# Optimization experiments

Measured on AMD Instinct MI355X. Metric: run time of the kernel, lower is better.

The kernel has to match this reference:

```python
import jax, jax.numpy as jnp
import numpy as np

N_HEAD = 16

def _rope_cos_sin(T, head_dim, dtype):
    # inv_freq over even indices, freqs [T, head_dim//2]
    inv_freq = 1.0 / (10000.0 ** (jnp.arange(0, head_dim, 2, dtype=jnp.float32) / head_dim))
    t = jnp.arange(T, dtype=jnp.float32)
    freqs = t[:, None] * inv_freq[None, :]
    cos = jnp.cos(freqs).astype(dtype)[None, :, None, :]  # [1,T,1,hd/2]
    sin = jnp.sin(freqs).astype(dtype)[None, :, None, :]
    return cos, sin

def _apply_rope(x, cos, sin):
    # x: [B,T,H,hd]; interleaved halves as in the torch module
    x1, x2 = x[..., ::2], x[..., 1::2]
    return jnp.concatenate([x1 * cos - x2 * sin, x1 * sin + x2 * cos], axis=-1)

def setup_inputs() -> dict:
    key = jax.random.key(0)
    k1, k2, k3 = jax.random.split(key, 3)
    B, T, C = 2, 2048, 1024
    x = jax.random.normal(k1, (B, T, C), dtype=jnp.float32)
    # causal mask (mask==0 positions get -inf), broadcast over B and heads
    attn_mask = jnp.tril(jnp.ones((T, T), dtype=bool))[None, None, :, :]
    w_qkv = jax.random.normal(k2, (C, 3 * C), dtype=jnp.float32) * (1.0 / np.sqrt(C))
    w_out = jax.random.normal(k3, (C, C), dtype=jnp.float32) * (1.0 / np.sqrt(C))
    return {"x": x, "attn_mask": attn_mask, "w_qkv": w_qkv, "w_out": w_out}

def reference(x, attn_mask, w_qkv, w_out):
    B, T, C = x.shape
    H = N_HEAD
    hd = C // H
    qkv = x @ w_qkv  # [B,T,3C]
    q, k, v = jnp.split(qkv, 3, axis=2)
    q = q.reshape(B, T, H, hd)
    k = k.reshape(B, T, H, hd)
    v = v.reshape(B, T, H, hd)
    cos, sin = _rope_cos_sin(T, hd, x.dtype)
    q = _apply_rope(q, cos, sin)
    k = _apply_rope(k, cos, sin)
    scale = 1.0 / np.sqrt(hd).astype(np.float32)
    att = jnp.einsum('bthd,bshd->bhts', q, k) * scale  # [B,H,T,T]
    att = jnp.where(attn_mask, att, -jnp.inf)
    att = jax.nn.softmax(att, axis=-1)
    out = jnp.einsum('bhts,bshd->bthd', att, v).reshape(B, T, C)
    out = out @ w_out
    k_t = jnp.transpose(k, (0, 2, 1, 3))  # [B,H,T,hd]
    v_t = jnp.transpose(v, (0, 2, 1, 3))
    return out, k_t, v_t
```

## Files before the change

kernel.cpp:

```cpp
#include <hip/hip_runtime.h>

#define T_SEQ 2048
#define NH    16
#define HD    64
#define CDIM  1024
#define BDIM  2

using floatx4 = __attribute__((ext_vector_type(4))) float;
using bf16x8  = __attribute__((ext_vector_type(8))) __bf16;
using half4   = __attribute__((ext_vector_type(4))) _Float16;
using half8   = __attribute__((ext_vector_type(8))) _Float16;
typedef unsigned short u16;

__device__ __forceinline__ u16 f2bf(float f) {
  unsigned int u = __float_as_uint(f);
  u += 0x7fffu + ((u >> 16) & 1u);
  return (u16)(u >> 16);
}
__device__ __forceinline__ float bf2f(u16 h) {
  return __uint_as_float(((unsigned int)h) << 16);
}
__device__ __forceinline__ u16 f2h(float f) {
  union { _Float16 h; u16 u; } c; c.h = (_Float16)f; return c.u;
}
__device__ __forceinline__ unsigned pk2h(float a, float b) {
  return __builtin_bit_cast(unsigned, __builtin_amdgcn_cvt_pkrtz(a, b));
}
__device__ __forceinline__ void gld16(const void* g, const void* l) {
  __builtin_amdgcn_global_load_lds(
      (const __attribute__((address_space(1))) unsigned int*)(unsigned long long)g,
      (__attribute__((address_space(3))) unsigned int*)(unsigned int)(unsigned long long)l,
      16, 0, 0);
}

__global__ __launch_bounds__(256) void preproc(const float* __restrict__ x,
                                               const float* __restrict__ w_qkv,
                                               const float* __restrict__ w_out,
                                               u16* __restrict__ xb,
                                               u16* __restrict__ wqT,
                                               u16* __restrict__ woT) {
  __shared__ float tile[32][33];
  int blk = blockIdx.x, tid = threadIdx.x;
  if (blk < 4096) {
    int i = blk * 256 + tid;
    float4 v = ((const float4*)x)[i];
    ushort4 o;
    o.x = f2bf(v.x); o.y = f2bf(v.y); o.z = f2bf(v.z); o.w = f2bf(v.w);
    ((ushort4*)xb)[i] = o;
    return;
  }
  const float* W; u16* WT; int K, N, bx, by;
  if (blk < 4096 + 3072) {
    int idx = blk - 4096; W = w_qkv; WT = wqT; K = 1024; N = 3072;
    bx = idx % 96; by = idx / 96;
  } else {
    int idx = blk - 7168; W = w_out; WT = woT; K = 1024; N = 1024;
    bx = idx & 31; by = idx >> 5;
  }
  int n0 = bx * 32, k0 = by * 32;
  int tx = tid & 31, ty = tid >> 5;
#pragma unroll
  for (int i = 0; i < 32; i += 8)
    tile[ty + i][tx] = W[(size_t)(k0 + ty + i) * N + n0 + tx];
  __syncthreads();
#pragma unroll
  for (int i = 0; i < 32; i += 8)
    WT[(size_t)(n0 + ty + i) * K + k0 + tx] = f2bf(tile[tx][ty + i]);
}

template <bool OUT_F32>
__global__ __launch_bounds__(256) void gemm_bt(const u16* __restrict__ A,
                                               const u16* __restrict__ BT,
                                               float* __restrict__ Cf,
                                               u16* __restrict__ Cb,
                                               int M, int N, int K) {
  __shared__ u16 As[2][128 * 32];
  __shared__ u16 Bs[2][128 * 32];
  const int tid  = threadIdx.x;
  const int lane = tid & 63, wave = tid >> 6;
  const int quad = lane >> 4, l16 = lane & 15;
  const int wm = (wave & 1) * 64, wn = (wave >> 1) * 64;
  const int row0 = blockIdx.x * 128, col0 = blockIdx.y * 128;
  const int srow = tid >> 2;
  const int sc   = tid & 3;
  const int sgc  = (sc ^ ((srow >> 1) & 3)) * 8;
  floatx4 acc[4][4] = {};

  auto stage = [&](int buf, int k0) {
    gld16(A  + (size_t)(row0 + srow     ) * K + k0 + sgc, &As[buf][srow * 32 + sc * 8]);
    gld16(A  + (size_t)(row0 + srow + 64) * K + k0 + sgc, &As[buf][(srow + 64) * 32 + sc * 8]);
    gld16(BT + (size_t)(col0 + srow     ) * K + k0 + sgc, &Bs[buf][srow * 32 + sc * 8]);
    gld16(BT + (size_t)(col0 + srow + 64) * K + k0 + sgc, &Bs[buf][(srow + 64) * 32 + sc * 8]);
  };

  const int nk = K >> 5;
  stage(0, 0);
  for (int ki = 0; ki < nk; ki++) {
    const int cur = ki & 1;
    __builtin_amdgcn_s_barrier();
    int kn = ki + 1 < nk ? ki + 1 : nk - 1;
    stage(cur ^ 1, kn << 5);
    asm volatile("s_waitcnt vmcnt(4)" ::: "memory");
    __builtin_amdgcn_s_barrier();
    bf16x8 af[4], bfv[4];
#pragma unroll
    for (int mt = 0; mt < 4; mt++) {
      int r = wm + mt * 16 + l16;
      af[mt] = *(const bf16x8*)&As[cur][r * 32 + (quad ^ ((r >> 1) & 3)) * 8];
    }
#pragma unroll
    for (int nt = 0; nt < 4; nt++) {
      int r = wn + nt * 16 + l16;
      bfv[nt] = *(const bf16x8*)&Bs[cur][r * 32 + (quad ^ ((r >> 1) & 3)) * 8];
    }
#pragma unroll
    for (int mt = 0; mt < 4; mt++)
#pragma unroll
      for (int nt = 0; nt < 4; nt++)
        acc[mt][nt] = __builtin_amdgcn_mfma_f32_16x16x32_bf16(af[mt], bfv[nt], acc[mt][nt], 0, 0, 0);
  }
  asm volatile("s_waitcnt vmcnt(0)" ::: "memory");
#pragma unroll
  for (int mt = 0; mt < 4; mt++)
#pragma unroll
    for (int nt = 0; nt < 4; nt++)
#pragma unroll
      for (int r = 0; r < 4; r++) {
        int row = row0 + wm + mt * 16 + quad * 4 + r;
        int col = col0 + wn + nt * 16 + l16;
        float v = acc[mt][nt][r];
        if (OUT_F32) Cf[(size_t)row * N + col] = v;
        else         Cb[(size_t)row * N + col] = f2bf(v);
      }
}

__global__ __launch_bounds__(256) void rope_vpack(const u16* __restrict__ qkv,
                                                  u16* __restrict__ qf16,
                                                  u16* __restrict__ kf16,
                                                  float* __restrict__ kt_out,
                                                  float* __restrict__ vt_out,
                                                  u16* __restrict__ vtf) {
  int blk = blockIdx.x;
  if (blk < 16384) {
    int gid = blk * 4 + (threadIdx.x >> 6);
    int d   = threadIdx.x & 63;
    int t   = gid & (T_SEQ - 1);
    int h   = (gid >> 11) & 15;
    int b   = gid >> 15;
    const u16* qrow = qkv + ((size_t)(b * T_SEQ + t)) * 3072 + h * 64;
    int i = d & 31;
    unsigned int qp = *(const unsigned int*)(qrow + 2 * i);
    unsigned int kp = *(const unsigned int*)(qrow + 1024 + 2 * i);
    float q1 = bf2f((u16)qp), q2 = bf2f((u16)(qp >> 16));
    float k1 = bf2f((u16)kp), k2 = bf2f((u16)(kp >> 16));
    float inv = expf((float)i * -0.28782313662425572f);
    float ang = (float)t * inv;
    float sn = sinf(ang), cs = cosf(ang);
    float qv = (d < 32) ? (q1 * cs - q2 * sn) : (q1 * sn + q2 * cs);
    float kv = (d < 32) ? (k1 * cs - k2 * sn) : (k1 * sn + k2 * cs);
    size_t o = (size_t)gid * 64 + d;
    qf16[o] = f2h(qv * 0.18033688011112042f);
    kf16[o] = f2h(kv);
    kt_out[o] = kv;
    return;
  }
  __shared__ float tile[64][65];
  int b2 = blk - 16384;
  int t0 = (b2 & 31) * 64;
  int bh = b2 >> 5;
  int b = bh >> 4, h = bh & 15;
  int tx = threadIdx.x & 63, ty = threadIdx.x >> 6;
#pragma unroll
  for (int i = ty; i < 64; i += 4) {
    float v = bf2f(qkv[((size_t)(b * T_SEQ + t0 + i)) * 3072 + 2048 + h * 64 + tx]);
    tile[i][tx] = v;
    vt_out[((size_t)bh * T_SEQ + t0 + i) * 64 + tx] = v;
  }
  __syncthreads();
#pragma unroll
  for (int i = ty; i < 64; i += 4)
    vtf[((size_t)bh * 64 + i) * T_SEQ + t0 + tx] = f2h(tile[tx][i]);
}

__device__ __forceinline__ void qk_dual(const u16* Ks, const half8* qfA, const half8* qfB,
                                        floatx4 (&sA)[8], floatx4 (&sB)[8],
                                        int quad, int l16) {
#pragma unroll
  for (int kc = 0; kc < 2; kc++)
#pragma unroll
    for (int st = 0; st < 8; st++) {
      int srow = st * 16 + l16;
      half8 ak = *(const half8*)&Ks[srow * 64 + (((kc * 4 + quad) ^ (srow & 7)) * 8)];
      sA[st] = __builtin_amdgcn_mfma_f32_16x16x32_f16(ak, qfA[kc], sA[st], 0, 0, 0);
      sB[st] = __builtin_amdgcn_mfma_f32_16x16x32_f16(ak, qfB[kc], sB[st], 0, 0, 0);
    }
}
__device__ __forceinline__ void qk_single(const u16* Ks, const half8* qfA,
                                          floatx4 (&sA)[8], int quad, int l16) {
#pragma unroll
  for (int kc = 0; kc < 2; kc++)
#pragma unroll
    for (int st = 0; st < 8; st++) {
      int srow = st * 16 + l16;
      half8 ak = *(const half8*)&Ks[srow * 64 + (((kc * 4 + quad) ^ (srow & 7)) * 8)];
      sA[st] = __builtin_amdgcn_mfma_f32_16x16x32_f16(ak, qfA[kc], sA[st], 0, 0, 0);
    }
}
__device__ __forceinline__ void apply_mask(floatx4 (&s)[8], int kt, int tw, int quad, int l16) {
  int tg = tw + l16;
#pragma unroll
  for (int st = 0; st < 8; st++) {
    int sg = kt * 128 + st * 16 + quad * 4;
#pragma unroll
    for (int r = 0; r < 4; r++)
      if (sg + r > tg) s[st][r] = -1e30f;
  }
}
__device__ __forceinline__ void softmax_update(floatx4 (&s)[8], float& mrow, float& lrow,
                                               floatx4 (&oacc)[4]) {
  floatx4 vm = s[0];
#pragma unroll
  for (int st = 1; st < 8; st++) {
    vm[0] = fmaxf(vm[0], s[st][0]); vm[1] = fmaxf(vm[1], s[st][1]);
    vm[2] = fmaxf(vm[2], s[st][2]); vm[3] = fmaxf(vm[3], s[st][3]);
  }
  float mx = fmaxf(fmaxf(vm[0], vm[1]), fmaxf(vm[2], vm[3]));
  mx = fmaxf(mx, __shfl_xor(mx, 16));
  mx = fmaxf(mx, __shfl_xor(mx, 32));
  if (!__all(mx <= mrow + 8.f)) {
    float mnew = fmaxf(mrow, mx);
    float alpha = exp2f(mrow - mnew);
    mrow = mnew;
    lrow *= alpha;
#pragma unroll
    for (int dt = 0; dt < 4; dt++) oacc[dt] *= alpha;
  }
  floatx4 vs = {0.f, 0.f, 0.f, 0.f};
#pragma unroll
  for (int st = 0; st < 8; st++) {
#pragma unroll
    for (int r = 0; r < 4; r++) s[st][r] = exp2f(s[st][r] - mrow);
    vs += s[st];
  }
  float rs = (vs[0] + vs[1]) + (vs[2] + vs[3]);
  rs += __shfl_xor(rs, 16);
  rs += __shfl_xor(rs, 32);
  lrow += rs;
}
__device__ __forceinline__ void pv_dual(const u16* Vts, const floatx4 (&sA)[8],
                                        const floatx4 (&sB)[8], floatx4 (&oA)[4],
                                        floatx4 (&oB)[4], int qh2, int ql2, int l16) {
#pragma unroll
  for (int st = 0; st < 8; st++) {
    union { unsigned u[2]; half4 h; } pa, pb;
    pa.u[0] = pk2h(sA[st][0], sA[st][1]); pa.u[1] = pk2h(sA[st][2], sA[st][3]);
    pb.u[0] = pk2h(sB[st][0], sB[st][1]); pb.u[1] = pk2h(sB[st][2], sB[st][3]);
#pragma unroll
    for (int dt = 0; dt < 4; dt++) {
      int drow = dt * 16 + l16;
      half4 av = *(const half4*)&Vts[drow * 128 + (((st * 2 + qh2) ^ (drow & 15)) * 8) + ql2];
      oA[dt] = __builtin_amdgcn_mfma_f32_16x16x16f16(av, pa.h, oA[dt], 0, 0, 0);
      oB[dt] = __builtin_amdgcn_mfma_f32_16x16x16f16(av, pb.h, oB[dt], 0, 0, 0);
    }
  }
}
__device__ __forceinline__ void pv_single(const u16* Vts, const floatx4 (&sA)[8],
                                          floatx4 (&oA)[4], int qh2, int ql2, int l16) {
#pragma unroll
  for (int st = 0; st < 8; st++) {
    union { unsigned u[2]; half4 h; } pa;
    pa.u[0] = pk2h(sA[st][0], sA[st][1]); pa.u[1] = pk2h(sA[st][2], sA[st][3]);
#pragma unroll
    for (int dt = 0; dt < 4; dt++) {
      int drow = dt * 16 + l16;
      half4 av = *(const half4*)&Vts[drow * 128 + (((st * 2 + qh2) ^ (drow & 15)) * 8) + ql2];
      oA[dt] = __builtin_amdgcn_mfma_f32_16x16x16f16(av, pa.h, oA[dt], 0, 0, 0);
    }
  }
}
__device__ __forceinline__ void epilogue(u16* __restrict__ Ob, const floatx4 (&oacc)[4],
                                         float lrow, int b, int h, int tw, int quad, int l16) {
  int t = tw + l16;
  float invl = 1.f / lrow;
#pragma unroll
  for (int dt = 0; dt < 4; dt++) {
    int d0 = dt * 16 + quad * 4;
    ushort4 o;
    o.x = f2bf(oacc[dt][0] * invl);
    o.y = f2bf(oacc[dt][1] * invl);
    o.z = f2bf(oacc[dt][2] * invl);
    o.w = f2bf(oacc[dt][3] * invl);
    *(ushort4*)&Ob[((size_t)(b * T_SEQ) + t) * CDIM + h * HD + d0] = o;
  }
}

__global__ __launch_bounds__(256, 2) void attn_fused(const u16* __restrict__ qf16,
                                                     const u16* __restrict__ kf16,
                                                     const u16* __restrict__ vtf,
                                                     u16* __restrict__ Ob) {
  __shared__ u16 Ks[2][128 * 64];
  __shared__ u16 Vts[2][64 * 128];
  const int tid = threadIdx.x;
  const int lane = tid & 63, wave = tid >> 6;
  const int quad = lane >> 4, l16 = lane & 15;
  const int qh2 = quad >> 1, ql2 = (quad & 1) * 4;
  const int j   = blockIdx.x >> 5;
  const int bh  = blockIdx.x & 31;
  const int b = bh >> 4, h = bh & 15;

  const int qtA = 31 - j, qtB = j;
  const int twA = qtA * 64 + wave * 16;
  const int twB = qtB * 64 + wave * 16;
  const int nktA = (qtA >> 1) + 1;
  const int nktB = (qtB >> 1) + 1;

  const u16* QgA = qf16 + ((size_t)bh * T_SEQ + twA) * HD;
  const u16* QgB = qf16 + ((size_t)bh * T_SEQ + twB) * HD;
  half8 qfA[2], qfB[2];
#pragma unroll
  for (int kc = 0; kc < 2; kc++) {
    qfA[kc] = *(const half8*)&QgA[(size_t)l16 * HD + kc * 32 + quad * 8];
    qfB[kc] = *(const half8*)&QgB[(size_t)l16 * HD + kc * 32 + quad * 8];
  }

  auto stage = [&](int buf, int kt) {
    const size_t koff = ((size_t)bh * T_SEQ + kt * 128) * HD;
    const u16* Vg = vtf + (size_t)bh * HD * T_SEQ + kt * 128;
    u16* Kd = &Ks[buf][0];
    u16* Vd = &Vts[buf][0];
#pragma unroll
    for (int jj = 0; jj < 4; jj++) {
      int t2 = jj * 256 + tid;
      int r = t2 >> 3, c = t2 & 7;
      gld16(kf16 + koff + r * HD + (c ^ (r & 7)) * 8, Kd + t2 * 8);
    }
#pragma unroll
    for (int jj = 0; jj < 4; jj++) {
      int t2 = jj * 256 + tid;
      int r = t2 >> 4, c = t2 & 15;
      gld16(Vg + (size_t)r * T_SEQ + (c ^ (r & 15)) * 8, Vd + t2 * 8);
    }
  };

  floatx4 oaccA[4] = {}, oaccB[4] = {};
  float mA = -1e30f, lA = 0.f;
  float mB = -1e30f, lB = 0.f;

  stage(0, 0);
#pragma unroll 1
  for (int kt = 0; kt < nktA; kt++) {
    const int cur = kt & 1;
    __builtin_amdgcn_s_barrier();
    int ktn = kt + 1 < nktA ? kt + 1 : nktA - 1;
    stage(cur ^ 1, ktn);
    asm volatile("s_waitcnt vmcnt(8)" ::: "memory");
    __builtin_amdgcn_s_barrier();
    const u16* Kc = &Ks[cur][0];
    const u16* Vc = &Vts[cur][0];

    if (kt < nktB) {
      floatx4 sA[8] = {}, sB[8] = {};
      qk_dual(Kc, qfA, qfB, sA, sB, quad, l16);
      if (kt == nktB - 1) apply_mask(sB, kt, twB, quad, l16);
      softmax_update(sA, mA, lA, oaccA);
      softmax_update(sB, mB, lB, oaccB);
      pv_dual(Vc, sA, sB, oaccA, oaccB, qh2, ql2, l16);
    } else {
      floatx4 sA[8] = {};
      qk_single(Kc, qfA, sA, quad, l16);
      if (kt == nktA - 1) apply_mask(sA, kt, twA, quad, l16);
      softmax_update(sA, mA, lA, oaccA);
      pv_single(Vc, sA, oaccA, qh2, ql2, l16);
    }
  }
  asm volatile("s_waitcnt vmcnt(0)" ::: "memory");
  epilogue(Ob, oaccA, lA, b, h, twA, quad, l16);
  epilogue(Ob, oaccB, lB, b, h, twB, quad, l16);
}

extern "C" void kernel_launch(void* const* d_in, const int* in_sizes, int n_in,
                              void* d_out, int out_size, void* d_ws, size_t ws_size,
                              hipStream_t stream) {
  const float* x     = (const float*)d_in[0];
  const float* w_qkv = (const float*)d_in[2];
  const float* w_out = (const float*)d_in[3];
  float* out    = (float*)d_out;
  float* kt_out = out + (size_t)BDIM * T_SEQ * CDIM;
  float* vt_out = kt_out + (size_t)BDIM * T_SEQ * CDIM;

  const size_t F = (size_t)4194304;
  char* base = (char*)d_ws;
  u16* xb   = (u16*)base;
  u16* wqT  = xb + F;
  u16* woT  = wqT + (size_t)3145728;
  u16* qkvb = woT + (size_t)1048576;
  u16* qf16 = qkvb + (size_t)3 * F;
  u16* kf16 = qf16 + F;
  u16* vtf  = (u16*)base;
  u16* Ob   = kf16 + F;

  preproc<<<8192, 256, 0, stream>>>(x, w_qkv, w_out, xb, wqT, woT);
  gemm_bt<false><<<dim3(32, 24), 256, 0, stream>>>(xb, wqT, (float*)nullptr, qkvb, 4096, 3072, 1024);
  rope_vpack<<<17408, 256, 0, stream>>>(qkvb, qf16, kf16, kt_out, vt_out, vtf);
  attn_fused<<<512, 256, 0, stream>>>(qf16, kf16, vtf, Ob);
  gemm_bt<true><<<dim3(32, 8), 256, 0, stream>>>(Ob, woT, out, (u16*)nullptr, 4096, 1024, 1024);
}
```

Baseline: 209.2 us.

## Compute softmax row sums via MFMA and drop K/V LDS double buffering

Row-sum accumulation for the online softmax moves from VALU adds plus cross-lane shuffles to an extra MFMA per tile against a ones vector, keeping the sum in an accumulator fragment. The K/V shared-memory staging goes from double-buffered with prefetch to a single buffer loaded synchronously between two __syncthreads. This halves LDS use, which may allow more resident blocks, but it gives up overlap of global loads with compute. The sum is now taken from fp16-rounded probabilities, which slightly changes the normalisation numerics.

```diff
diff --git a/kernel.cpp b/kernel.cpp
--- a/kernel.cpp
+++ b/kernel.cpp
@@ -216,45 +216,43 @@
       if (sg + r > tg) s[st][r] = -1e30f;
   }
 }
-__device__ __forceinline__ void softmax_update(floatx4 (&s)[8], float& mrow, float& lrow,
-                                               floatx4 (&oacc)[4]) {
-  floatx4 vm = s[0];
-#pragma unroll
-  for (int st = 1; st < 8; st++) {
-    vm[0] = fmaxf(vm[0], s[st][0]); vm[1] = fmaxf(vm[1], s[st][1]);
-    vm[2] = fmaxf(vm[2], s[st][2]); vm[3] = fmaxf(vm[3], s[st][3]);
-  }
-  float mx = fmaxf(fmaxf(vm[0], vm[1]), fmaxf(vm[2], vm[3]));
+__device__ __forceinline__ float vmax4(const floatx4& v) {
+  return fmaxf(fmaxf(fmaxf(v[0], v[1]), v[2]), v[3]);
+}
+__device__ __forceinline__ void softmax_update(floatx4 (&s)[8], float& mrow,
+                                               floatx4& lsum, floatx4 (&oacc)[4]) {
+  float p0 = fmaxf(vmax4(s[0]), vmax4(s[1]));
+  float p1 = fmaxf(vmax4(s[2]), vmax4(s[3]));
+  float p2 = fmaxf(vmax4(s[4]), vmax4(s[5]));
+  float p3 = fmaxf(vmax4(s[6]), vmax4(s[7]));
+  float mx = fmaxf(fmaxf(fmaxf(p0, p1), p2), p3);
   mx = fmaxf(mx, __shfl_xor(mx, 16));
   mx = fmaxf(mx, __shfl_xor(mx, 32));
   if (!__all(mx <= mrow + 8.f)) {
     float mnew = fmaxf(mrow, mx);
     float alpha = exp2f(mrow - mnew);
     mrow = mnew;
-    lrow *= alpha;
+    lsum *= alpha;
 #pragma unroll
     for (int dt = 0; dt < 4; dt++) oacc[dt] *= alpha;
   }
-  floatx4 vs = {0.f, 0.f, 0.f, 0.f};
-#pragma unroll
-  for (int st = 0; st < 8; st++) {
+#pragma unroll
+  for (int st = 0; st < 8; st++)
 #pragma unroll
     for (int r = 0; r < 4; r++) s[st][r] = exp2f(s[st][r] - mrow);
-    vs += s[st];
-  }
-  float rs = (vs[0] + vs[1]) + (vs[2] + vs[3]);
-  rs += __shfl_xor(rs, 16);
-  rs += __shfl_xor(rs, 32);
-  lrow += rs;
 }
 __device__ __forceinline__ void pv_dual(const u16* Vts, const floatx4 (&sA)[8],
                                         const floatx4 (&sB)[8], floatx4 (&oA)[4],
-                                        floatx4 (&oB)[4], int qh2, int ql2, int l16) {
+                                        floatx4 (&oB)[4], floatx4& lsA, floatx4& lsB,
+                                        int qh2, int ql2, int l16) {
+  const half4 vones = {(_Float16)1.f, (_Float16)1.f, (_Float16)1.f, (_Float16)1.f};
 #pragma unroll
   for (int st = 0; st < 8; st++) {
     union { unsigned u[2]; half4 h; } pa, pb;
     pa.u[0] = pk2h(sA[st][0], sA[st][1]); pa.u[1] = pk2h(sA[st][2], sA[st][3]);
     pb.u[0] = pk2h(sB[st][0], sB[st][1]); pb.u[1] = pk2h(sB[st][2], sB[st][3]);
+    lsA = __builtin_amdgcn_mfma_f32_16x16x16f16(vones, pa.h, lsA, 0, 0, 0);
+    lsB = __builtin_amdgcn_mfma_f32_16x16x16f16(vones, pb.h, lsB, 0, 0, 0);
 #pragma unroll
     for (int dt = 0; dt < 4; dt++) {
       int drow = dt * 16 + l16;
@@ -265,11 +263,14 @@
   }
 }
 __device__ __forceinline__ void pv_single(const u16* Vts, const floatx4 (&sA)[8],
-                                          floatx4 (&oA)[4], int qh2, int ql2, int l16) {
+                                          floatx4 (&oA)[4], floatx4& lsA,
+                                          int qh2, int ql2, int l16) {
+  const half4 vones = {(_Float16)1.f, (_Float16)1.f, (_Float16)1.f, (_Float16)1.f};
 #pragma unroll
   for (int st = 0; st < 8; st++) {
     union { unsigned u[2]; half4 h; } pa;
     pa.u[0] = pk2h(sA[st][0], sA[st][1]); pa.u[1] = pk2h(sA[st][2], sA[st][3]);
+    lsA = __builtin_amdgcn_mfma_f32_16x16x16f16(vones, pa.h, lsA, 0, 0, 0);
 #pragma unroll
     for (int dt = 0; dt < 4; dt++) {
       int drow = dt * 16 + l16;
@@ -279,9 +280,10 @@
   }
 }
 __device__ __forceinline__ void epilogue(u16* __restrict__ Ob, const floatx4 (&oacc)[4],
-                                         float lrow, int b, int h, int tw, int quad, int l16) {
+                                         const floatx4& lsum, int b, int h, int tw,
+                                         int quad, int l16) {
   int t = tw + l16;
-  float invl = 1.f / lrow;
+  float invl = 1.f / lsum[0];
 #pragma unroll
   for (int dt = 0; dt < 4; dt++) {
     int d0 = dt * 16 + quad * 4;
@@ -298,8 +300,8 @@
                                                      const u16* __restrict__ kf16,
                                                      const u16* __restrict__ vtf,
                                                      u16* __restrict__ Ob) {
-  __shared__ u16 Ks[2][128 * 64];
-  __shared__ u16 Vts[2][64 * 128];
+  __shared__ u16 Ks[128 * 64];
+  __shared__ u16 Vts[64 * 128];
   const int tid = threadIdx.x;
   const int lane = tid & 63, wave = tid >> 6;
   const int quad = lane >> 4, l16 = lane & 15;
@@ -323,59 +325,46 @@
     qfB[kc] = *(const half8*)&QgB[(size_t)l16 * HD + kc * 32 + quad * 8];
   }
 
-  auto stage = [&](int buf, int kt) {
+  floatx4 oaccA[4] = {}, oaccB[4] = {};
+  floatx4 lsA = {}, lsB = {};
+  float mA = -1e30f, mB = -1e30f;
+
+#pragma unroll 1
+  for (int kt = 0; kt < nktA; kt++) {
+    __syncthreads();
     const size_t koff = ((size_t)bh * T_SEQ + kt * 128) * HD;
     const u16* Vg = vtf + (size_t)bh * HD * T_SEQ + kt * 128;
-    u16* Kd = &Ks[buf][0];
-    u16* Vd = &Vts[buf][0];
 #pragma unroll
     for (int jj = 0; jj < 4; jj++) {
       int t2 = jj * 256 + tid;
       int r = t2 >> 3, c = t2 & 7;
-      gld16(kf16 + koff + r * HD + (c ^ (r & 7)) * 8, Kd + t2 * 8);
+      gld16(kf16 + koff + r * HD + (c ^ (r & 7)) * 8, &Ks[t2 * 8]);
     }
 #pragma unroll
     for (int jj = 0; jj < 4; jj++) {
       int t2 = jj * 256 + tid;
       int r = t2 >> 4, c = t2 & 15;
-      gld16(Vg + (size_t)r * T_SEQ + (c ^ (r & 15)) * 8, Vd + t2 * 8);
-    }
-  };
-
-  floatx4 oaccA[4] = {}, oaccB[4] = {};
-  float mA = -1e30f, lA = 0.f;
-  float mB = -1e30f, lB = 0.f;
-
-  stage(0, 0);
-#pragma unroll 1
-  for (int kt = 0; kt < nktA; kt++) {
-    const int cur = kt & 1;
-    __builtin_amdgcn_s_barrier();
-    int ktn = kt + 1 < nktA ? kt + 1 : nktA - 1;
-    stage(cur ^ 1, ktn);
-    asm volatile("s_waitcnt vmcnt(8)" ::: "memory");
-    __builtin_amdgcn_s_barrier();
-    const u16* Kc = &Ks[cur][0];
-    const u16* Vc = &Vts[cur][0];
+      gld16(Vg + (size_t)r * T_SEQ + (c ^ (r & 15)) * 8, &Vts[t2 * 8]);
+    }
+    __syncthreads();
 
     if (kt < nktB) {
       floatx4 sA[8] = {}, sB[8] = {};
-      qk_dual(Kc, qfA, qfB, sA, sB, quad, l16);
+      qk_dual(Ks, qfA, qfB, sA, sB, quad, l16);
       if (kt == nktB - 1) apply_mask(sB, kt, twB, quad, l16);
-      softmax_update(sA, mA, lA, oaccA);
-      softmax_update(sB, mB, lB, oaccB);
-      pv_dual(Vc, sA, sB, oaccA, oaccB, qh2, ql2, l16);
+      softmax_update(sA, mA, lsA, oaccA);
+      softmax_update(sB, mB, lsB, oaccB);
+      pv_dual(Vts, sA, sB, oaccA, oaccB, lsA, lsB, qh2, ql2, l16);
     } else {
       floatx4 sA[8] = {};
-      qk_single(Kc, qfA, sA, quad, l16);
+      qk_single(Ks, qfA, sA, quad, l16);
       if (kt == nktA - 1) apply_mask(sA, kt, twA, quad, l16);
-      softmax_update(sA, mA, lA, oaccA);
-      pv_single(Vc, sA, oaccA, qh2, ql2, l16);
-    }
-  }
-  asm volatile("s_waitcnt vmcnt(0)" ::: "memory");
-  epilogue(Ob, oaccA, lA, b, h, twA, quad, l16);
-  epilogue(Ob, oaccB, lB, b, h, twB, quad, l16);
+      softmax_update(sA, mA, lsA, oaccA);
+      pv_single(Vts, sA, oaccA, lsA, qh2, ql2, l16);
+    }
+  }
+  epilogue(Ob, oaccA, lsA, b, h, twA, quad, l16);
+  epilogue(Ob, oaccB, lsB, b, h, twB, quad, l16);
 }
 
 extern "C" void kernel_launch(void* const* d_in, const int* in_sizes, int n_in,
```

Measured after the change: 208.3 us. Within noise of the previous version (-0.5%).
